# Kernel optimization log

Measured on AMD Instinct MI355X. Metric: run time of the kernel, lower is better.

## Reference

```python
import jax, jax.numpy as jnp
import numpy as np
import math

N_HEADS = 8

def setup_inputs() -> dict:
    key = jax.random.key(0)
    qkv = jax.random.normal(key, (2, 1536, 4096), dtype=jnp.float32)
    return {"qkv": qkv}

def reference(qkv):
    bs, width, length = qkv.shape
    ch = width // (3 * N_HEADS)
    # [bs*H, 3*ch, T] -> split into q, k, v each [bs*H, ch, T]
    qkv_r = qkv.reshape(bs * N_HEADS, 3 * ch, length)
    q, k, v = jnp.split(qkv_r, 3, axis=1)
    scale = 1.0 / math.sqrt(math.sqrt(ch))
    # scores [b, t, s]
    weight = jnp.einsum('bct,bcs->bts', q * scale, k * scale)
    weight = jax.nn.softmax(weight.astype(jnp.float32), axis=-1).astype(weight.dtype)
    a = jnp.einsum('bts,bcs->bct', weight, v)
    return a.reshape(bs, N_HEADS * ch, length)
```

## Files before the change

### kernel.cpp

```cpp
#include <hip/hip_runtime.h>

#define TSEQ 4096
#define QB   128
#define KB   64
#define NTT  (TSEQ / KB)
#define NTG  (NTT / 2)

typedef __attribute__((ext_vector_type(16))) float f32x16;
typedef __attribute__((ext_vector_type(8)))  short bf16x8;
typedef __attribute__((ext_vector_type(4)))  unsigned uint4v;

union Frag { unsigned u[4]; bf16x8 v; };

static __device__ __forceinline__ unsigned cvt_pk(float lo, float hi) {
  unsigned r;
  asm("v_cvt_pk_bf16_f32 %0, %1, %2" : "=v"(r) : "v"(lo), "v"(hi));
  return r;
}

static __device__ __forceinline__ void gload16(const void* g, void* l) {
  __builtin_amdgcn_global_load_lds(
      (const __attribute__((address_space(1))) unsigned*)g,
      (__attribute__((address_space(3))) unsigned*)l, 16, 0, 0);
}

static __device__ __forceinline__ void decode_attn(int hw, int& bh, int& sub) {
  const int xcd = hw & 7, slot = hw >> 3;
  bh  = xcd * 2 + (slot >> 5);
  sub = slot & 31;
}
static __device__ __forceinline__ void decode_pre(int hw, int& bh, int& sub) {
  const int xcd = hw & 7, slot = hw >> 3;
  bh  = xcd * 2 + (slot >> 6);
  sub = slot & 63;
}

__global__ __launch_bounds__(256)
void preconvert_kernel(const float* __restrict__ qkv,
                       unsigned short* __restrict__ kimg,
                       unsigned short* __restrict__ vimg) {
  int bh, tile;
  decode_pre(blockIdx.x, bh, tile);
  const int bsI  = bh >> 3;
  const int head = bh & 7;
  const size_t base = ((size_t)bsI * 1536 + (size_t)head * 192) * TSEQ;
  const float* __restrict__ Kg = qkv + base + (size_t)64  * TSEQ;
  const float* __restrict__ Vg = qkv + base + (size_t)128 * TSEQ;
  const int s0 = tile * KB;
  const int t  = threadIdx.x;
  const size_t tb = (size_t)(bh * NTT + tile) * 8192;

  {
    const int s = t & 63;
    char* kout = (char*)kimg + tb + (size_t)s * 128;
    const unsigned swz = (unsigned)((s & 7) << 4);
#pragma unroll
    for (int q = 0; q < 2; ++q) {
      const int cc = (t >> 6) + q * 4;
      float f[8];
#pragma unroll
      for (int j = 0; j < 8; ++j)
        f[j] = Kg[(size_t)(8 * cc + j) * TSEQ + s0 + s];
      uint4v d = { cvt_pk(f[0], f[1]), cvt_pk(f[2], f[3]),
                   cvt_pk(f[4], f[5]), cvt_pk(f[6], f[7]) };
      *(uint4v*)(kout + (((unsigned)(cc << 4)) ^ swz)) = d;
    }
  }

  {
    const int c  = t >> 2;
    const int sb = (t & 3) * 16;
    const float* src = &Vg[(size_t)c * TSEQ + s0 + sb];
    const float4 a0 = ((const float4*)src)[0];
    const float4 a1 = ((const float4*)src)[1];
    const float4 a2 = ((const float4*)src)[2];
    const float4 a3 = ((const float4*)src)[3];
    char* vout = (char*)vimg + tb + (size_t)c * 128;
    const unsigned cswz = (unsigned)((c & 7) << 4);
    const int ss = (t & 3) * 2;
    uint4v d0 = { cvt_pk(a0.x, a0.y), cvt_pk(a0.z, a0.w),
                  cvt_pk(a1.x, a1.y), cvt_pk(a1.z, a1.w) };
    uint4v d1 = { cvt_pk(a2.x, a2.y), cvt_pk(a2.z, a2.w),
                  cvt_pk(a3.x, a3.y), cvt_pk(a3.z, a3.w) };
    *(uint4v*)(vout + (((unsigned)(ss << 4)) ^ cswz))       = d0;
    *(uint4v*)(vout + (((unsigned)((ss + 1) << 4)) ^ cswz)) = d1;
  }
}

__global__ __launch_bounds__(512, 4)
void qkv_attn_kernel(const float* __restrict__ qkv,
                     const unsigned short* __restrict__ kimg,
                     const unsigned short* __restrict__ vimg,
                     float* __restrict__ out) {
  __shared__ __align__(16) unsigned short Kt[2][2][KB * 64];
  __shared__ __align__(16) unsigned short Vt[2][2][64 * KB];

  const int tid  = threadIdx.x;
  const int w    = tid >> 6;
  const int g    = w >> 2;
  const int wg   = w & 3;
  const int lane = tid & 63;
  const int h    = lane >> 5;
  const int ln   = lane & 31;

  int bh, qt;
  decode_attn(blockIdx.x, bh, qt);
  const int bsI  = bh >> 3;
  const int head = bh & 7;

  const size_t base = ((size_t)bsI * 1536 + (size_t)head * 192) * TSEQ;
  const float* __restrict__ Qg = qkv + base;

  const int tq = qt * QB + wg * 32 + ln;

  const float QSCALE = 0.125f * 1.44269504088896340736f;

  const size_t hb = (size_t)bh * NTT * 8192;
  const char* __restrict__ kim = (const char*)kimg + hb + wg * 2048 + lane * 16;
  const char* __restrict__ vim = (const char*)vimg + hb + wg * 2048 + lane * 16;

#define STAGE(buf, tile)                                                    \
  {                                                                         \
    const size_t o = (size_t)(g * NTG + (tile)) * 8192;                     \
    char* kl = (char*)(&Kt[g][buf][0]) + wg * 2048;                         \
    char* vl = (char*)(&Vt[g][buf][0]) + wg * 2048;                         \
    gload16(kim + o, kl);                                                   \
    gload16(kim + o + 1024, kl + 1024);                                    \
    gload16(vim + o, vl);                                                   \
    gload16(vim + o + 1024, vl + 1024);                                    \
  }

  STAGE(0, 0);

  Frag qf[4];
#pragma unroll
  for (int ks = 0; ks < 4; ++ks) {
#pragma unroll
    for (int p = 0; p < 4; ++p) {
      const int c = ks * 16 + h * 8 + 2 * p;
      const float a = Qg[(size_t)c * TSEQ + tq] * QSCALE;
      const float b = Qg[(size_t)(c + 1) * TSEQ + tq] * QSCALE;
      qf[ks].u[p] = cvt_pk(a, b);
    }
  }

  f32x16 acc0 = {0,0,0,0,0,0,0,0,0,0,0,0,0,0,0,0};
  f32x16 acc1 = {0,0,0,0,0,0,0,0,0,0,0,0,0,0,0,0};
  float lrun = 0.0f;

  for (int it = 0; it < NTG; ++it) {
    const int cur = it & 1;

    if (it + 1 < NTG) {
      STAGE(cur ^ 1, it + 1);
      asm volatile("s_waitcnt vmcnt(4)" ::: "memory");
    } else {
      asm volatile("s_waitcnt vmcnt(0)" ::: "memory");
    }
    __builtin_amdgcn_s_barrier();
    __builtin_amdgcn_sched_barrier(0);

    const char* kbase = (const char*)(&Kt[g][cur][0]);
    const char* vbase = (const char*)(&Vt[g][cur][0]);

    f32x16 sc0 = {0,0,0,0,0,0,0,0,0,0,0,0,0,0,0,0};
    f32x16 sc1 = {0,0,0,0,0,0,0,0,0,0,0,0,0,0,0,0};
    __builtin_amdgcn_s_setprio(1);
#pragma unroll
    for (int ks = 0; ks < 4; ++ks) {
      const int coff2 = (ks * 16 + h * 8) * 2;
      const int sA = ln, sB = 32 + ln;
      const bf16x8 kA = *(const bf16x8*)(kbase + sA * 128 + (coff2 ^ ((sA & 7) << 4)));
      const bf16x8 kB = *(const bf16x8*)(kbase + sB * 128 + (coff2 ^ ((sB & 7) << 4)));
      sc0 = __builtin_amdgcn_mfma_f32_32x32x16_bf16(kA, qf[ks].v, sc0, 0, 0, 0);
      sc1 = __builtin_amdgcn_mfma_f32_32x32x16_bf16(kB, qf[ks].v, sc1, 0, 0, 0);
    }
    __builtin_amdgcn_s_setprio(0);

    float ssum = 0.0f;
#pragma unroll
    for (int r = 0; r < 16; ++r) {
      const float p0 = __builtin_amdgcn_exp2f(sc0[r]);
      const float p1 = __builtin_amdgcn_exp2f(sc1[r]);
      sc0[r] = p0; sc1[r] = p1;
      ssum += p0 + p1;
    }
    ssum += __shfl_xor(ssum, 32);
    lrun += ssum;

    Frag pf[4];
#pragma unroll
    for (int mt = 0; mt < 2; ++mt) {
      const f32x16& s = mt ? sc1 : sc0;
      unsigned A0 = cvt_pk(s[0],  s[1]),  A1 = cvt_pk(s[2],  s[3]);
      unsigned B0 = cvt_pk(s[4],  s[5]),  B1 = cvt_pk(s[6],  s[7]);
      unsigned C0 = cvt_pk(s[8],  s[9]),  C1 = cvt_pk(s[10], s[11]);
      unsigned D0 = cvt_pk(s[12], s[13]), D1 = cvt_pk(s[14], s[15]);
      asm("v_permlane32_swap_b32 %0, %1" : "+v"(A0), "+v"(B0));
      asm("v_permlane32_swap_b32 %0, %1" : "+v"(A1), "+v"(B1));
      asm("v_permlane32_swap_b32 %0, %1" : "+v"(C0), "+v"(D0));
      asm("v_permlane32_swap_b32 %0, %1" : "+v"(C1), "+v"(D1));
      pf[2 * mt + 0].u[0] = A0; pf[2 * mt + 0].u[1] = A1;
      pf[2 * mt + 0].u[2] = B0; pf[2 * mt + 0].u[3] = B1;
      pf[2 * mt + 1].u[0] = C0; pf[2 * mt + 1].u[1] = C1;
      pf[2 * mt + 1].u[2] = D0; pf[2 * mt + 1].u[3] = D1;
    }

    __builtin_amdgcn_s_setprio(1);
#pragma unroll
    for (int ks = 0; ks < 4; ++ks) {
      const int soff2 = (ks * 16 + h * 8) * 2;
      const int cA = ln, cB = 32 + ln;
      const bf16x8 vA = *(const bf16x8*)(vbase + cA * 128 + (soff2 ^ ((cA & 7) << 4)));
      const bf16x8 vB = *(const bf16x8*)(vbase + cB * 128 + (soff2 ^ ((cB & 7) << 4)));
      acc0 = __builtin_amdgcn_mfma_f32_32x32x16_bf16(vA, pf[ks].v, acc0, 0, 0, 0);
      acc1 = __builtin_amdgcn_mfma_f32_32x32x16_bf16(vB, pf[ks].v, acc1, 0, 0, 0);
    }
    __builtin_amdgcn_s_setprio(0);

    __builtin_amdgcn_sched_barrier(0);
    __builtin_amdgcn_s_barrier();
  }

  float* exch0 = (float*)(&Kt[0][0][0]);
  float* exch1 = (float*)(&Vt[0][0][0]);
  float* lex   = (float*)((char*)(&Vt[0][0][0]) + 20480);
  const int t0 = tid & 255;

  if (g == 1) {
#pragma unroll
    for (int r = 0; r < 16; ++r) {
      exch0[t0 * 17 + r] = acc0[r];
      exch1[t0 * 17 + r] = acc1[r];
    }
    lex[t0] = lrun;
  }
  __syncthreads();
  if (g == 0) {
    const float linv = 1.0f / (lrun + lex[t0]);
    const size_t obase = ((size_t)bsI * 512 + (size_t)head * 64) * TSEQ + tq;
#pragma unroll
    for (int r = 0; r < 16; ++r) {
      const int crow = (r & 3) + 8 * (r >> 2) + 4 * h;
      out[obase + (size_t)crow * TSEQ] =
          (acc0[r] + exch0[t0 * 17 + r]) * linv;
      out[obase + (size_t)(crow + 32) * TSEQ] =
          (acc1[r] + exch1[t0 * 17 + r]) * linv;
    }
  }
}

extern "C" void kernel_launch(void* const* d_in, const int* in_sizes, int n_in,
                              void* d_out, int out_size, void* d_ws, size_t ws_size,
                              hipStream_t stream) {
  const float* qkv = (const float*)d_in[0];
  float* out = (float*)d_out;
  (void)in_sizes; (void)n_in; (void)out_size; (void)ws_size;

  unsigned short* kimg = (unsigned short*)d_ws;
  unsigned short* vimg = (unsigned short*)((char*)d_ws + 8388608);

  hipLaunchKernelGGL(preconvert_kernel, dim3(16 * NTT), dim3(256), 0, stream,
                     qkv, kimg, vimg);
  hipLaunchKernelGGL(qkv_attn_kernel, dim3(16 * (TSEQ / QB)), dim3(512), 0,
                     stream, qkv, kimg, vimg, out);
}
```

Before: 94.41 us.

## Software-pipeline PV matmul one tile behind QK with triple-buffered V

Result: no change. 94.31 us (-0.1%).

```diff
diff --git a/kernel.cpp b/kernel.cpp
--- a/kernel.cpp
+++ b/kernel.cpp
@@ -93,7 +93,7 @@
                      const unsigned short* __restrict__ vimg,
                      float* __restrict__ out) {
   __shared__ __align__(16) unsigned short Kt[2][2][KB * 64];
-  __shared__ __align__(16) unsigned short Vt[2][2][64 * KB];
+  __shared__ __align__(16) unsigned short Vt[2][3][64 * KB];
 
   const int tid  = threadIdx.x;
   const int w    = tid >> 6;
@@ -119,18 +119,23 @@
   const char* __restrict__ kim = (const char*)kimg + hb + wg * 2048 + lane * 16;
   const char* __restrict__ vim = (const char*)vimg + hb + wg * 2048 + lane * 16;
 
-#define STAGE(buf, tile)                                                    \
+#define STAGE_K(kbuf, tile)                                                 \
   {                                                                         \
     const size_t o = (size_t)(g * NTG + (tile)) * 8192;                     \
-    char* kl = (char*)(&Kt[g][buf][0]) + wg * 2048;                         \
-    char* vl = (char*)(&Vt[g][buf][0]) + wg * 2048;                         \
+    char* kl = (char*)(&Kt[g][kbuf][0]) + wg * 2048;                        \
     gload16(kim + o, kl);                                                   \
-    gload16(kim + o + 1024, kl + 1024);                                    \
+    gload16(kim + o + 1024, kl + 1024);                                     \
+  }
+#define STAGE_V(vslot, tile)                                                \
+  {                                                                         \
+    const size_t o = (size_t)(g * NTG + (tile)) * 8192;                     \
+    char* vl = (char*)(&Vt[g][vslot][0]) + wg * 2048;                       \
     gload16(vim + o, vl);                                                   \
-    gload16(vim + o + 1024, vl + 1024);                                    \
-  }
-
-  STAGE(0, 0);
+    gload16(vim + o + 1024, vl + 1024);                                     \
+  }
+
+  STAGE_K(0, 0);
+  STAGE_V(0, 0);
 
   Frag qf[4];
 #pragma unroll
@@ -147,12 +152,15 @@
   f32x16 acc0 = {0,0,0,0,0,0,0,0,0,0,0,0,0,0,0,0};
   f32x16 acc1 = {0,0,0,0,0,0,0,0,0,0,0,0,0,0,0,0};
   float lrun = 0.0f;
+  Frag pfp[4];
+
+  int wp = 1;
+  int rp = 0;
 
   for (int it = 0; it < NTG; ++it) {
-    const int cur = it & 1;
-
     if (it + 1 < NTG) {
-      STAGE(cur ^ 1, it + 1);
+      STAGE_K((it + 1) & 1, it + 1);
+      STAGE_V(wp, it + 1);
       asm volatile("s_waitcnt vmcnt(4)" ::: "memory");
     } else {
       asm volatile("s_waitcnt vmcnt(0)" ::: "memory");
@@ -160,8 +168,7 @@
     __builtin_amdgcn_s_barrier();
     __builtin_amdgcn_sched_barrier(0);
 
-    const char* kbase = (const char*)(&Kt[g][cur][0]);
-    const char* vbase = (const char*)(&Vt[g][cur][0]);
+    const char* kbase = (const char*)(&Kt[g][it & 1][0]);
 
     f32x16 sc0 = {0,0,0,0,0,0,0,0,0,0,0,0,0,0,0,0};
     f32x16 sc1 = {0,0,0,0,0,0,0,0,0,0,0,0,0,0,0,0};
@@ -177,18 +184,32 @@
     }
     __builtin_amdgcn_s_setprio(0);
 
-    float ssum = 0.0f;
+    if (it > 0) {
+      const char* vbase = (const char*)(&Vt[g][rp][0]);
+      __builtin_amdgcn_s_setprio(1);
+#pragma unroll
+      for (int ks = 0; ks < 4; ++ks) {
+        const int soff2 = (ks * 16 + h * 8) * 2;
+        const int cA = ln, cB = 32 + ln;
+        const bf16x8 vA = *(const bf16x8*)(vbase + cA * 128 + (soff2 ^ ((cA & 7) << 4)));
+        const bf16x8 vB = *(const bf16x8*)(vbase + cB * 128 + (soff2 ^ ((cB & 7) << 4)));
+        acc0 = __builtin_amdgcn_mfma_f32_32x32x16_bf16(vA, pfp[ks].v, acc0, 0, 0, 0);
+        acc1 = __builtin_amdgcn_mfma_f32_32x32x16_bf16(vB, pfp[ks].v, acc1, 0, 0, 0);
+      }
+      __builtin_amdgcn_s_setprio(0);
+      rp = (rp + 1 == 3) ? 0 : rp + 1;
+    }
+
+    float lsum = 0.0f;
 #pragma unroll
     for (int r = 0; r < 16; ++r) {
       const float p0 = __builtin_amdgcn_exp2f(sc0[r]);
       const float p1 = __builtin_amdgcn_exp2f(sc1[r]);
       sc0[r] = p0; sc1[r] = p1;
-      ssum += p0 + p1;
-    }
-    ssum += __shfl_xor(ssum, 32);
-    lrun += ssum;
-
-    Frag pf[4];
+      lsum += p0 + p1;
+    }
+    lrun += lsum;
+
 #pragma unroll
     for (int mt = 0; mt < 2; ++mt) {
       const f32x16& s = mt ? sc1 : sc0;
@@ -200,12 +221,19 @@
       asm("v_permlane32_swap_b32 %0, %1" : "+v"(A1), "+v"(B1));
       asm("v_permlane32_swap_b32 %0, %1" : "+v"(C0), "+v"(D0));
       asm("v_permlane32_swap_b32 %0, %1" : "+v"(C1), "+v"(D1));
-      pf[2 * mt + 0].u[0] = A0; pf[2 * mt + 0].u[1] = A1;
-      pf[2 * mt + 0].u[2] = B0; pf[2 * mt + 0].u[3] = B1;
-      pf[2 * mt + 1].u[0] = C0; pf[2 * mt + 1].u[1] = C1;
-      pf[2 * mt + 1].u[2] = D0; pf[2 * mt + 1].u[3] = D1;
-    }
-
+      pfp[2 * mt + 0].u[0] = A0; pfp[2 * mt + 0].u[1] = A1;
+      pfp[2 * mt + 0].u[2] = B0; pfp[2 * mt + 0].u[3] = B1;
+      pfp[2 * mt + 1].u[0] = C0; pfp[2 * mt + 1].u[1] = C1;
+      pfp[2 * mt + 1].u[2] = D0; pfp[2 * mt + 1].u[3] = D1;
+    }
+
+    __builtin_amdgcn_sched_barrier(0);
+    __builtin_amdgcn_s_barrier();
+    wp = (wp + 1 == 3) ? 0 : wp + 1;
+  }
+
+  {
+    const char* vbase = (const char*)(&Vt[g][(NTG - 1) % 3][0]);
     __builtin_amdgcn_s_setprio(1);
 #pragma unroll
     for (int ks = 0; ks < 4; ++ks) {
@@ -213,15 +241,14 @@
       const int cA = ln, cB = 32 + ln;
       const bf16x8 vA = *(const bf16x8*)(vbase + cA * 128 + (soff2 ^ ((cA & 7) << 4)));
       const bf16x8 vB = *(const bf16x8*)(vbase + cB * 128 + (soff2 ^ ((cB & 7) << 4)));
-      acc0 = __builtin_amdgcn_mfma_f32_32x32x16_bf16(vA, pf[ks].v, acc0, 0, 0, 0);
-      acc1 = __builtin_amdgcn_mfma_f32_32x32x16_bf16(vB, pf[ks].v, acc1, 0, 0, 0);
+      acc0 = __builtin_amdgcn_mfma_f32_32x32x16_bf16(vA, pfp[ks].v, acc0, 0, 0, 0);
+      acc1 = __builtin_amdgcn_mfma_f32_32x32x16_bf16(vB, pfp[ks].v, acc1, 0, 0, 0);
     }
     __builtin_amdgcn_s_setprio(0);
-
-    __builtin_amdgcn_sched_barrier(0);
-    __builtin_amdgcn_s_barrier();
-  }
-
+  }
+  lrun += __shfl_xor(lrun, 32);
+
+  __syncthreads();
   float* exch0 = (float*)(&Kt[0][0][0]);
   float* exch1 = (float*)(&Vt[0][0][0]);
   float* lex   = (float*)((char*)(&Vt[0][0][0]) + 20480);
```

## Load K fragments directly into registers from MFMA-ordered global image

Applied to the files above, without the earlier changes.

Measured after the change: 101.3 us. 7.3% more time.

```diff
diff --git a/kernel.cpp b/kernel.cpp
--- a/kernel.cpp
+++ b/kernel.cpp
@@ -10,7 +10,7 @@
 typedef __attribute__((ext_vector_type(8)))  short bf16x8;
 typedef __attribute__((ext_vector_type(4)))  unsigned uint4v;
 
-union Frag { unsigned u[4]; bf16x8 v; };
+union Frag { unsigned u[4]; uint4v q; bf16x8 v; };
 
 static __device__ __forceinline__ unsigned cvt_pk(float lo, float hi) {
   unsigned r;
@@ -50,21 +50,20 @@
   const int t  = threadIdx.x;
   const size_t tb = (size_t)(bh * NTT + tile) * 8192;
 
-  {
-    const int s = t & 63;
-    char* kout = (char*)kimg + tb + (size_t)s * 128;
-    const unsigned swz = (unsigned)((s & 7) << 4);
-#pragma unroll
-    for (int q = 0; q < 2; ++q) {
-      const int cc = (t >> 6) + q * 4;
-      float f[8];
-#pragma unroll
-      for (int j = 0; j < 8; ++j)
-        f[j] = Kg[(size_t)(8 * cc + j) * TSEQ + s0 + s];
-      uint4v d = { cvt_pk(f[0], f[1]), cvt_pk(f[2], f[3]),
-                   cvt_pk(f[4], f[5]), cvt_pk(f[6], f[7]) };
-      *(uint4v*)(kout + (((unsigned)(cc << 4)) ^ swz)) = d;
-    }
+#pragma unroll
+  for (int q = 0; q < 2; ++q) {
+    const int p  = t + 256 * q;
+    const int f  = p >> 6;
+    const int l  = p & 63;
+    const int ks = f >> 1, mt = f & 1;
+    const int hh = l >> 5, ll = l & 31;
+    float fl[8];
+#pragma unroll
+    for (int j = 0; j < 8; ++j)
+      fl[j] = Kg[(size_t)(ks * 16 + hh * 8 + j) * TSEQ + s0 + mt * 32 + ll];
+    uint4v d = { cvt_pk(fl[0], fl[1]), cvt_pk(fl[2], fl[3]),
+                 cvt_pk(fl[4], fl[5]), cvt_pk(fl[6], fl[7]) };
+    *(uint4v*)((char*)kimg + tb + f * 1024 + l * 16) = d;
   }
 
   {
@@ -92,8 +91,8 @@
                      const unsigned short* __restrict__ kimg,
                      const unsigned short* __restrict__ vimg,
                      float* __restrict__ out) {
-  __shared__ __align__(16) unsigned short Kt[2][2][KB * 64];
   __shared__ __align__(16) unsigned short Vt[2][2][64 * KB];
+  __shared__ __align__(16) float ex[256 * 35];
 
   const int tid  = threadIdx.x;
   const int w    = tid >> 6;
@@ -116,21 +115,32 @@
   const float QSCALE = 0.125f * 1.44269504088896340736f;
 
   const size_t hb = (size_t)bh * NTT * 8192;
-  const char* __restrict__ kim = (const char*)kimg + hb + wg * 2048 + lane * 16;
+  const char* __restrict__ kim = (const char*)kimg + hb + lane * 16;
   const char* __restrict__ vim = (const char*)vimg + hb + wg * 2048 + lane * 16;
 
-#define STAGE(buf, tile)                                                    \
+#define STAGE_V(buf, tile)                                                  \
   {                                                                         \
     const size_t o = (size_t)(g * NTG + (tile)) * 8192;                     \
-    char* kl = (char*)(&Kt[g][buf][0]) + wg * 2048;                         \
     char* vl = (char*)(&Vt[g][buf][0]) + wg * 2048;                         \
-    gload16(kim + o, kl);                                                   \
-    gload16(kim + o + 1024, kl + 1024);                                    \
     gload16(vim + o, vl);                                                   \
-    gload16(vim + o + 1024, vl + 1024);                                    \
-  }
-
-  STAGE(0, 0);
+    gload16(vim + o + 1024, vl + 1024);                                     \
+  }
+#define LOADK(tile)                                                         \
+  {                                                                         \
+    const char* tp = kim + (size_t)(g * NTG + (tile)) * 8192;               \
+    kf[0].q = *(const uint4v*)(tp);                                         \
+    kf[1].q = *(const uint4v*)(tp + 1024);                                  \
+    kf[2].q = *(const uint4v*)(tp + 2048);                                  \
+    kf[3].q = *(const uint4v*)(tp + 3072);                                  \
+    kf[4].q = *(const uint4v*)(tp + 4096);                                  \
+    kf[5].q = *(const uint4v*)(tp + 5120);                                  \
+    kf[6].q = *(const uint4v*)(tp + 6144);                                  \
+    kf[7].q = *(const uint4v*)(tp + 7168);                                  \
+  }
+
+  Frag kf[8];
+  LOADK(0);
+  STAGE_V(0, 0);
 
   Frag qf[4];
 #pragma unroll
@@ -152,41 +162,36 @@
     const int cur = it & 1;
 
     if (it + 1 < NTG) {
-      STAGE(cur ^ 1, it + 1);
-      asm volatile("s_waitcnt vmcnt(4)" ::: "memory");
+      STAGE_V(cur ^ 1, it + 1);
+      asm volatile("s_waitcnt vmcnt(2)" ::: "memory");
     } else {
       asm volatile("s_waitcnt vmcnt(0)" ::: "memory");
     }
     __builtin_amdgcn_s_barrier();
     __builtin_amdgcn_sched_barrier(0);
-
-    const char* kbase = (const char*)(&Kt[g][cur][0]);
-    const char* vbase = (const char*)(&Vt[g][cur][0]);
 
     f32x16 sc0 = {0,0,0,0,0,0,0,0,0,0,0,0,0,0,0,0};
     f32x16 sc1 = {0,0,0,0,0,0,0,0,0,0,0,0,0,0,0,0};
     __builtin_amdgcn_s_setprio(1);
 #pragma unroll
     for (int ks = 0; ks < 4; ++ks) {
-      const int coff2 = (ks * 16 + h * 8) * 2;
-      const int sA = ln, sB = 32 + ln;
-      const bf16x8 kA = *(const bf16x8*)(kbase + sA * 128 + (coff2 ^ ((sA & 7) << 4)));
-      const bf16x8 kB = *(const bf16x8*)(kbase + sB * 128 + (coff2 ^ ((sB & 7) << 4)));
-      sc0 = __builtin_amdgcn_mfma_f32_32x32x16_bf16(kA, qf[ks].v, sc0, 0, 0, 0);
-      sc1 = __builtin_amdgcn_mfma_f32_32x32x16_bf16(kB, qf[ks].v, sc1, 0, 0, 0);
+      sc0 = __builtin_amdgcn_mfma_f32_32x32x16_bf16(kf[2 * ks + 0].v, qf[ks].v, sc0, 0, 0, 0);
+      sc1 = __builtin_amdgcn_mfma_f32_32x32x16_bf16(kf[2 * ks + 1].v, qf[ks].v, sc1, 0, 0, 0);
     }
     __builtin_amdgcn_s_setprio(0);
-
-    float ssum = 0.0f;
+    __builtin_amdgcn_sched_barrier(0);
+
+    if (it + 1 < NTG) LOADK(it + 1);
+
+    float lsum = 0.0f;
 #pragma unroll
     for (int r = 0; r < 16; ++r) {
       const float p0 = __builtin_amdgcn_exp2f(sc0[r]);
       const float p1 = __builtin_amdgcn_exp2f(sc1[r]);
       sc0[r] = p0; sc1[r] = p1;
-      ssum += p0 + p1;
-    }
-    ssum += __shfl_xor(ssum, 32);
-    lrun += ssum;
+      lsum += p0 + p1;
+    }
+    lrun += lsum;
 
     Frag pf[4];
 #pragma unroll
@@ -206,6 +211,7 @@
       pf[2 * mt + 1].u[2] = D0; pf[2 * mt + 1].u[3] = D1;
     }
 
+    const char* vbase = (const char*)(&Vt[g][cur][0]);
     __builtin_amdgcn_s_setprio(1);
 #pragma unroll
     for (int ks = 0; ks < 4; ++ks) {
@@ -222,30 +228,29 @@
     __builtin_amdgcn_s_barrier();
   }
 
-  float* exch0 = (float*)(&Kt[0][0][0]);
-  float* exch1 = (float*)(&Vt[0][0][0]);
-  float* lex   = (float*)((char*)(&Vt[0][0][0]) + 20480);
+  lrun += __shfl_xor(lrun, 32);
+
+  __syncthreads();
   const int t0 = tid & 255;
-
   if (g == 1) {
 #pragma unroll
     for (int r = 0; r < 16; ++r) {
-      exch0[t0 * 17 + r] = acc0[r];
-      exch1[t0 * 17 + r] = acc1[r];
-    }
-    lex[t0] = lrun;
+      ex[t0 * 35 + r]      = acc0[r];
+      ex[t0 * 35 + 16 + r] = acc1[r];
+    }
+    ex[t0 * 35 + 34] = lrun;
   }
   __syncthreads();
   if (g == 0) {
-    const float linv = 1.0f / (lrun + lex[t0]);
+    const float linv = 1.0f / (lrun + ex[t0 * 35 + 34]);
     const size_t obase = ((size_t)bsI * 512 + (size_t)head * 64) * TSEQ + tq;
 #pragma unroll
     for (int r = 0; r < 16; ++r) {
       const int crow = (r & 3) + 8 * (r >> 2) + 4 * h;
       out[obase + (size_t)crow * TSEQ] =
-          (acc0[r] + exch0[t0 * 17 + r]) * linv;
+          (acc0[r] + ex[t0 * 35 + r]) * linv;
       out[obase + (size_t)(crow + 32) * TSEQ] =
-          (acc1[r] + exch1[t0 * 17 + r]) * linv;
+          (acc1[r] + ex[t0 * 35 + 16 + r]) * linv;
     }
   }
 }
```

## Split KV halves across separate blocks with global partials and combine kernel

Applied to the files above, without the earlier changes.

New measurement: 101.0 us. 1.07x slower.

```diff
diff --git a/kernel.cpp b/kernel.cpp
--- a/kernel.cpp
+++ b/kernel.cpp
@@ -24,12 +24,12 @@
       (__attribute__((address_space(3))) unsigned*)l, 16, 0, 0);
 }
 
-static __device__ __forceinline__ void decode_attn(int hw, int& bh, int& sub) {
+static __device__ __forceinline__ void decode512(int hw, int& bh, int& sub) {
   const int xcd = hw & 7, slot = hw >> 3;
   bh  = xcd * 2 + (slot >> 5);
   sub = slot & 31;
 }
-static __device__ __forceinline__ void decode_pre(int hw, int& bh, int& sub) {
+static __device__ __forceinline__ void decode1024(int hw, int& bh, int& sub) {
   const int xcd = hw & 7, slot = hw >> 3;
   bh  = xcd * 2 + (slot >> 6);
   sub = slot & 63;
@@ -40,7 +40,7 @@
                        unsigned short* __restrict__ kimg,
                        unsigned short* __restrict__ vimg) {
   int bh, tile;
-  decode_pre(blockIdx.x, bh, tile);
+  decode1024(blockIdx.x, bh, tile);
   const int bsI  = bh >> 3;
   const int head = bh & 7;
   const size_t base = ((size_t)bsI * 1536 + (size_t)head * 192) * TSEQ;
@@ -66,7 +66,6 @@
       *(uint4v*)(kout + (((unsigned)(cc << 4)) ^ swz)) = d;
     }
   }
-
   {
     const int c  = t >> 2;
     const int sb = (t & 3) * 16;
@@ -87,141 +86,236 @@
   }
 }
 
-__global__ __launch_bounds__(512, 4)
-void qkv_attn_kernel(const float* __restrict__ qkv,
-                     const unsigned short* __restrict__ kimg,
-                     const unsigned short* __restrict__ vimg,
-                     float* __restrict__ out) {
-  __shared__ __align__(16) unsigned short Kt[2][2][KB * 64];
-  __shared__ __align__(16) unsigned short Vt[2][2][64 * KB];
+#define ATTN_LOOP(NITER, TBASE, KTARR, VTARR, WIDX)                          \
+  for (int it = 0; it < (NITER); ++it) {                                     \
+    const int cur = it & 1;                                                  \
+    if (it + 1 < (NITER)) {                                                  \
+      const size_t o = (size_t)((TBASE) + it + 1) * 8192;                    \
+      char* kl = (char*)(&KTARR[cur ^ 1][0]) + (WIDX) * 2048;                \
+      char* vl = (char*)(&VTARR[cur ^ 1][0]) + (WIDX) * 2048;                \
+      gload16(kimP + o, kl);                                                 \
+      gload16(kimP + o + 1024, kl + 1024);                                   \
+      gload16(vimP + o, vl);                                                 \
+      gload16(vimP + o + 1024, vl + 1024);                                   \
+      asm volatile("s_waitcnt vmcnt(4)" ::: "memory");                       \
+    } else {                                                                 \
+      asm volatile("s_waitcnt vmcnt(0)" ::: "memory");                       \
+    }                                                                        \
+    __builtin_amdgcn_s_barrier();                                            \
+    __builtin_amdgcn_sched_barrier(0);                                       \
+    const char* kbase = (const char*)(&KTARR[cur][0]);                       \
+    const char* vbase = (const char*)(&VTARR[cur][0]);                       \
+    f32x16 sc0 = {0,0,0,0,0,0,0,0,0,0,0,0,0,0,0,0};                          \
+    f32x16 sc1 = {0,0,0,0,0,0,0,0,0,0,0,0,0,0,0,0};                          \
+    __builtin_amdgcn_s_setprio(1);                                           \
+    _Pragma("unroll")                                                        \
+    for (int ks = 0; ks < 4; ++ks) {                                         \
+      const int coff2 = (ks * 16 + h * 8) * 2;                               \
+      const int sA = ln, sB = 32 + ln;                                       \
+      const bf16x8 kA = *(const bf16x8*)(kbase + sA * 128 +                  \
+                                         (coff2 ^ ((sA & 7) << 4)));         \
+      const bf16x8 kB = *(const bf16x8*)(kbase + sB * 128 +                  \
+                                         (coff2 ^ ((sB & 7) << 4)));         \
+      sc0 = __builtin_amdgcn_mfma_f32_32x32x16_bf16(kA, qf[ks].v, sc0,0,0,0);\
+      sc1 = __builtin_amdgcn_mfma_f32_32x32x16_bf16(kB, qf[ks].v, sc1,0,0,0);\
+    }                                                                        \
+    __builtin_amdgcn_s_setprio(0);                                           \
+    float lsum = 0.0f;                                                       \
+    _Pragma("unroll")                                                        \
+    for (int r = 0; r < 16; ++r) {                                           \
+      const float p0 = __builtin_amdgcn_exp2f(sc0[r]);                       \
+      const float p1 = __builtin_amdgcn_exp2f(sc1[r]);                       \
+      sc0[r] = p0; sc1[r] = p1;                                              \
+      lsum += p0 + p1;                                                       \
+    }                                                                        \
+    lrun += lsum;                                                            \
+    Frag pf[4];                                                              \
+    _Pragma("unroll")                                                        \
+    for (int mt = 0; mt < 2; ++mt) {                                         \
+      const f32x16& s = mt ? sc1 : sc0;                                      \
+      unsigned A0 = cvt_pk(s[0],  s[1]),  A1 = cvt_pk(s[2],  s[3]);          \
+      unsigned B0 = cvt_pk(s[4],  s[5]),  B1 = cvt_pk(s[6],  s[7]);          \
+      unsigned C0 = cvt_pk(s[8],  s[9]),  C1 = cvt_pk(s[10], s[11]);         \
+      unsigned D0 = cvt_pk(s[12], s[13]), D1 = cvt_pk(s[14], s[15]);         \
+      asm("v_permlane32_swap_b32 %0, %1" : "+v"(A0), "+v"(B0));              \
+      asm("v_permlane32_swap_b32 %0, %1" : "+v"(A1), "+v"(B1));              \
+      asm("v_permlane32_swap_b32 %0, %1" : "+v"(C0), "+v"(D0));              \
+      asm("v_permlane32_swap_b32 %0, %1" : "+v"(C1), "+v"(D1));              \
+      pf[2 * mt + 0].u[0] = A0; pf[2 * mt + 0].u[1] = A1;                    \
+      pf[2 * mt + 0].u[2] = B0; pf[2 * mt + 0].u[3] = B1;                    \
+      pf[2 * mt + 1].u[0] = C0; pf[2 * mt + 1].u[1] = C1;                    \
+      pf[2 * mt + 1].u[2] = D0; pf[2 * mt + 1].u[3] = D1;                    \
+    }                                                                        \
+    __builtin_amdgcn_s_setprio(1);                                           \
+    _Pragma("unroll")                                                        \
+    for (int ks = 0; ks < 4; ++ks) {                                         \
+      const int soff2 = (ks * 16 + h * 8) * 2;                               \
+      const int cA = ln, cB = 32 + ln;                                       \
+      const bf16x8 vA = *(const bf16x8*)(vbase + cA * 128 +                  \
+                                         (soff2 ^ ((cA & 7) << 4)));         \
+      const bf16x8 vB = *(const bf16x8*)(vbase + cB * 128 +                  \
+                                         (soff2 ^ ((cB & 7) << 4)));         \
+      acc0 = __builtin_amdgcn_mfma_f32_32x32x16_bf16(vA, pf[ks].v, acc0,0,0,0);\
+      acc1 = __builtin_amdgcn_mfma_f32_32x32x16_bf16(vB, pf[ks].v, acc1,0,0,0);\
+    }                                                                        \
+    __builtin_amdgcn_s_setprio(0);                                           \
+    __builtin_amdgcn_sched_barrier(0);                                       \
+    __builtin_amdgcn_s_barrier();                                            \
+  }
+
+#define BUILD_QF()                                                           \
+  Frag qf[4];                                                                \
+  _Pragma("unroll")                                                          \
+  for (int ks = 0; ks < 4; ++ks) {                                           \
+    _Pragma("unroll")                                                        \
+    for (int p = 0; p < 4; ++p) {                                            \
+      const int c = ks * 16 + h * 8 + 2 * p;                                 \
+      const float a = Qg[(size_t)c * TSEQ + tq] * QSCALE;                    \
+      const float b = Qg[(size_t)(c + 1) * TSEQ + tq] * QSCALE;              \
+      qf[ks].u[p] = cvt_pk(a, b);                                            \
+    }                                                                        \
+  }
+
+__global__ __launch_bounds__(256, 4)
+void qkv_attn_half_kernel(const float* __restrict__ qkv,
+                          const unsigned short* __restrict__ kimg,
+                          const unsigned short* __restrict__ vimg,
+                          float* __restrict__ part) {
+  __shared__ __align__(16) unsigned short Kt[2][KB * 64];
+  __shared__ __align__(16) unsigned short Vt[2][64 * KB];
 
   const int tid  = threadIdx.x;
   const int w    = tid >> 6;
-  const int g    = w >> 2;
-  const int wg   = w & 3;
   const int lane = tid & 63;
   const int h    = lane >> 5;
   const int ln   = lane & 31;
 
-  int bh, qt;
-  decode_attn(blockIdx.x, bh, qt);
+  int bh, sub;
+  decode1024(blockIdx.x, bh, sub);
+  const int qt   = sub >> 1;
+  const int half = sub & 1;
   const int bsI  = bh >> 3;
   const int head = bh & 7;
 
   const size_t base = ((size_t)bsI * 1536 + (size_t)head * 192) * TSEQ;
   const float* __restrict__ Qg = qkv + base;
-
-  const int tq = qt * QB + wg * 32 + ln;
-
+  const int tq = qt * QB + w * 32 + ln;
   const float QSCALE = 0.125f * 1.44269504088896340736f;
 
   const size_t hb = (size_t)bh * NTT * 8192;
-  const char* __restrict__ kim = (const char*)kimg + hb + wg * 2048 + lane * 16;
-  const char* __restrict__ vim = (const char*)vimg + hb + wg * 2048 + lane * 16;
-
-#define STAGE(buf, tile)                                                    \
-  {                                                                         \
-    const size_t o = (size_t)(g * NTG + (tile)) * 8192;                     \
-    char* kl = (char*)(&Kt[g][buf][0]) + wg * 2048;                         \
-    char* vl = (char*)(&Vt[g][buf][0]) + wg * 2048;                         \
-    gload16(kim + o, kl);                                                   \
-    gload16(kim + o + 1024, kl + 1024);                                    \
-    gload16(vim + o, vl);                                                   \
-    gload16(vim + o + 1024, vl + 1024);                                    \
-  }
-
-  STAGE(0, 0);
-
-  Frag qf[4];
-#pragma unroll
-  for (int ks = 0; ks < 4; ++ks) {
-#pragma unroll
-    for (int p = 0; p < 4; ++p) {
-      const int c = ks * 16 + h * 8 + 2 * p;
-      const float a = Qg[(size_t)c * TSEQ + tq] * QSCALE;
-      const float b = Qg[(size_t)(c + 1) * TSEQ + tq] * QSCALE;
-      qf[ks].u[p] = cvt_pk(a, b);
-    }
-  }
+  const char* __restrict__ kimP = (const char*)kimg + hb + w * 2048 + lane * 16;
+  const char* __restrict__ vimP = (const char*)vimg + hb + w * 2048 + lane * 16;
+
+  {
+    const size_t o = (size_t)(half * NTG) * 8192;
+    char* kl = (char*)(&Kt[0][0]) + w * 2048;
+    char* vl = (char*)(&Vt[0][0]) + w * 2048;
+    gload16(kimP + o, kl);
+    gload16(kimP + o + 1024, kl + 1024);
+    gload16(vimP + o, vl);
+    gload16(vimP + o + 1024, vl + 1024);
+  }
+
+  BUILD_QF();
 
   f32x16 acc0 = {0,0,0,0,0,0,0,0,0,0,0,0,0,0,0,0};
   f32x16 acc1 = {0,0,0,0,0,0,0,0,0,0,0,0,0,0,0,0};
   float lrun = 0.0f;
 
-  for (int it = 0; it < NTG; ++it) {
-    const int cur = it & 1;
-
-    if (it + 1 < NTG) {
-      STAGE(cur ^ 1, it + 1);
-      asm volatile("s_waitcnt vmcnt(4)" ::: "memory");
-    } else {
-      asm volatile("s_waitcnt vmcnt(0)" ::: "memory");
-    }
-    __builtin_amdgcn_s_barrier();
-    __builtin_amdgcn_sched_barrier(0);
-
-    const char* kbase = (const char*)(&Kt[g][cur][0]);
-    const char* vbase = (const char*)(&Vt[g][cur][0]);
-
-    f32x16 sc0 = {0,0,0,0,0,0,0,0,0,0,0,0,0,0,0,0};
-    f32x16 sc1 = {0,0,0,0,0,0,0,0,0,0,0,0,0,0,0,0};
-    __builtin_amdgcn_s_setprio(1);
-#pragma unroll
-    for (int ks = 0; ks < 4; ++ks) {
-      const int coff2 = (ks * 16 + h * 8) * 2;
-      const int sA = ln, sB = 32 + ln;
-      const bf16x8 kA = *(const bf16x8*)(kbase + sA * 128 + (coff2 ^ ((sA & 7) << 4)));
-      const bf16x8 kB = *(const bf16x8*)(kbase + sB * 128 + (coff2 ^ ((sB & 7) << 4)));
-      sc0 = __builtin_amdgcn_mfma_f32_32x32x16_bf16(kA, qf[ks].v, sc0, 0, 0, 0);
-      sc1 = __builtin_amdgcn_mfma_f32_32x32x16_bf16(kB, qf[ks].v, sc1, 0, 0, 0);
-    }
-    __builtin_amdgcn_s_setprio(0);
-
-    float ssum = 0.0f;
-#pragma unroll
-    for (int r = 0; r < 16; ++r) {
-      const float p0 = __builtin_amdgcn_exp2f(sc0[r]);
-      const float p1 = __builtin_amdgcn_exp2f(sc1[r]);
-      sc0[r] = p0; sc1[r] = p1;
-      ssum += p0 + p1;
-    }
-    ssum += __shfl_xor(ssum, 32);
-    lrun += ssum;
-
-    Frag pf[4];
-#pragma unroll
-    for (int mt = 0; mt < 2; ++mt) {
-      const f32x16& s = mt ? sc1 : sc0;
-      unsigned A0 = cvt_pk(s[0],  s[1]),  A1 = cvt_pk(s[2],  s[3]);
-      unsigned B0 = cvt_pk(s[4],  s[5]),  B1 = cvt_pk(s[6],  s[7]);
-      unsigned C0 = cvt_pk(s[8],  s[9]),  C1 = cvt_pk(s[10], s[11]);
-      unsigned D0 = cvt_pk(s[12], s[13]), D1 = cvt_pk(s[14], s[15]);
-      asm("v_permlane32_swap_b32 %0, %1" : "+v"(A0), "+v"(B0));
-      asm("v_permlane32_swap_b32 %0, %1" : "+v"(A1), "+v"(B1));
-      asm("v_permlane32_swap_b32 %0, %1" : "+v"(C0), "+v"(D0));
-      asm("v_permlane32_swap_b32 %0, %1" : "+v"(C1), "+v"(D1));
-      pf[2 * mt + 0].u[0] = A0; pf[2 * mt + 0].u[1] = A1;
-      pf[2 * mt + 0].u[2] = B0; pf[2 * mt + 0].u[3] = B1;
-      pf[2 * mt + 1].u[0] = C0; pf[2 * mt + 1].u[1] = C1;
-      pf[2 * mt + 1].u[2] = D0; pf[2 * mt + 1].u[3] = D1;
-    }
-
-    __builtin_amdgcn_s_setprio(1);
-#pragma unroll
-    for (int ks = 0; ks < 4; ++ks) {
-      const int soff2 = (ks * 16 + h * 8) * 2;
-      const int cA = ln, cB = 32 + ln;
-      const bf16x8 vA = *(const bf16x8*)(vbase + cA * 128 + (soff2 ^ ((cA & 7) << 4)));
-      const bf16x8 vB = *(const bf16x8*)(vbase + cB * 128 + (soff2 ^ ((cB & 7) << 4)));
-      acc0 = __builtin_amdgcn_mfma_f32_32x32x16_bf16(vA, pf[ks].v, acc0, 0, 0, 0);
-      acc1 = __builtin_amdgcn_mfma_f32_32x32x16_bf16(vB, pf[ks].v, acc1, 0, 0, 0);
-    }
-    __builtin_amdgcn_s_setprio(0);
-
-    __builtin_amdgcn_sched_barrier(0);
-    __builtin_amdgcn_s_barrier();
-  }
-
+  ATTN_LOOP(NTG, half * NTG, Kt, Vt, w);
+
+  lrun += __shfl_xor(lrun, 32);
+
+  float* pb = part + (size_t)blockIdx.x * (33 * 256);
+#pragma unroll
+  for (int r = 0; r < 16; ++r) {
+    pb[r * 256 + tid]        = acc0[r];
+    pb[(16 + r) * 256 + tid] = acc1[r];
+  }
+  pb[32 * 256 + tid] = lrun;
+}
+
+__global__ __launch_bounds__(256)
+void combine_kernel(const float* __restrict__ part, float* __restrict__ out) {
+  int bh, qt;
+  decode512(blockIdx.x, bh, qt);
+  const int bsI  = bh >> 3;
+  const int head = bh & 7;
+  const int t    = threadIdx.x;
+  const int w    = t >> 6;
+  const int lane = t & 63;
+  const int h    = lane >> 5;
+  const int ln   = lane & 31;
+  const int tq   = qt * QB + w * 32 + ln;
+
+  const int hw0 = (((bh & 1) * 64 + qt * 2 + 0) << 3) + (bh >> 1);
+  const int hw1 = (((bh & 1) * 64 + qt * 2 + 1) << 3) + (bh >> 1);
+  const float* p0 = part + (size_t)hw0 * (33 * 256);
+  const float* p1 = part + (size_t)hw1 * (33 * 256);
+
+  const float linv = 1.0f / (p0[32 * 256 + t] + p1[32 * 256 + t]);
+  const size_t obase = ((size_t)bsI * 512 + (size_t)head * 64) * TSEQ + tq;
+#pragma unroll
+  for (int r = 0; r < 16; ++r) {
+    const int crow = (r & 3) + 8 * (r >> 2) + 4 * h;
+    const float a0 = p0[r * 256 + t]        + p1[r * 256 + t];
+    const float a1 = p0[(16 + r) * 256 + t] + p1[(16 + r) * 256 + t];
+    out[obase + (size_t)crow * TSEQ]        = a0 * linv;
+    out[obase + (size_t)(crow + 32) * TSEQ] = a1 * linv;
+  }
+}
+
+__global__ __launch_bounds__(512, 4)
+void qkv_attn_full_kernel(const float* __restrict__ qkv,
+                          const unsigned short* __restrict__ kimg,
+                          const unsigned short* __restrict__ vimg,
+                          float* __restrict__ out) {
+  __shared__ __align__(16) unsigned short Kt[2][2][KB * 64];
+  __shared__ __align__(16) unsigned short Vt[2][2][64 * KB];
+
+  const int tid  = threadIdx.x;
+  const int wv   = tid >> 6;
+  const int g    = wv >> 2;
+  const int wg   = wv & 3;
+  const int lane = tid & 63;
+  const int h    = lane >> 5;
+  const int ln   = lane & 31;
+
+  int bh, qt;
+  decode512(blockIdx.x, bh, qt);
+  const int bsI  = bh >> 3;
+  const int head = bh & 7;
+
+  const size_t base = ((size_t)bsI * 1536 + (size_t)head * 192) * TSEQ;
+  const float* __restrict__ Qg = qkv + base;
+  const int tq = qt * QB + wg * 32 + ln;
+  const float QSCALE = 0.125f * 1.44269504088896340736f;
+
+  const size_t hb = (size_t)bh * NTT * 8192;
+  const char* __restrict__ kimP = (const char*)kimg + hb + wg * 2048 + lane * 16;
+  const char* __restrict__ vimP = (const char*)vimg + hb + wg * 2048 + lane * 16;
+
+  {
+    const size_t o = (size_t)(g * NTG) * 8192;
+    char* kl = (char*)(&Kt[g][0][0]) + wg * 2048;
+    char* vl = (char*)(&Vt[g][0][0]) + wg * 2048;
+    gload16(kimP + o, kl);
+    gload16(kimP + o + 1024, kl + 1024);
+    gload16(vimP + o, vl);
+    gload16(vimP + o + 1024, vl + 1024);
+  }
+
+  BUILD_QF();
+
+  f32x16 acc0 = {0,0,0,0,0,0,0,0,0,0,0,0,0,0,0,0};
+  f32x16 acc1 = {0,0,0,0,0,0,0,0,0,0,0,0,0,0,0,0};
+  float lrun = 0.0f;
+
+  ATTN_LOOP(NTG, g * NTG, Kt[g], Vt[g], wg);
+
+  lrun += __shfl_xor(lrun, 32);
+
+  __syncthreads();
   float* exch0 = (float*)(&Kt[0][0][0]);
   float* exch1 = (float*)(&Vt[0][0][0]);
   float* lex   = (float*)((char*)(&Vt[0][0][0]) + 20480);
@@ -255,13 +349,22 @@
                               hipStream_t stream) {
   const float* qkv = (const float*)d_in[0];
   float* out = (float*)d_out;
-  (void)in_sizes; (void)n_in; (void)out_size; (void)ws_size;
+  (void)in_sizes; (void)n_in; (void)out_size;
 
   unsigned short* kimg = (unsigned short*)d_ws;
   unsigned short* vimg = (unsigned short*)((char*)d_ws + 8388608);
+  float* part = (float*)((char*)d_ws + 16777216);
+  const size_t need = 16777216 + (size_t)1024 * 33 * 256 * 4;
 
   hipLaunchKernelGGL(preconvert_kernel, dim3(16 * NTT), dim3(256), 0, stream,
                      qkv, kimg, vimg);
-  hipLaunchKernelGGL(qkv_attn_kernel, dim3(16 * (TSEQ / QB)), dim3(512), 0,
-                     stream, qkv, kimg, vimg, out);
-}
+  if (ws_size >= need) {
+    hipLaunchKernelGGL(qkv_attn_half_kernel, dim3(1024), dim3(256), 0, stream,
+                       qkv, kimg, vimg, part);
+    hipLaunchKernelGGL(combine_kernel, dim3(512), dim3(256), 0, stream,
+                       part, out);
+  } else {
+    hipLaunchKernelGGL(qkv_attn_full_kernel, dim3(512), dim3(512), 0, stream,
+                       qkv, kimg, vimg, out);
+  }
+}
```
